# Kernel tuning notes

Measured on AMD Instinct MI355X. Metric: run time of the kernel, lower is better.

The kernel has to match this reference:

```python
import jax, jax.numpy as jnp
import numpy as np

SEQ_LEN = 8192
HIDDEN = 4096
QMAX = 127.0


def _quantize(x_f, scale):
    # per-position requant: round(x / scale), clip to int8 range
    return jnp.clip(jnp.round(x_f / scale[:, None]), -QMAX, QMAX)


def setup_inputs() -> dict:
    key = jax.random.key(0)
    k1, k2, k3, k4 = jax.random.split(key, 4)
    # int8-valued input in [-127, 127]
    x = jax.random.randint(k1, (SEQ_LEN, HIDDEN), -127, 128, dtype=jnp.int32).astype(jnp.int8)
    # per-position scales (calibrated buffers); small positive values typical of int8 activations
    scale_x = jax.random.uniform(k2, (SEQ_LEN,), jnp.float32, 0.01, 0.05)
    scale_y = jax.random.uniform(k3, (SEQ_LEN,), jnp.float32, 0.005, 0.01)  # sigmoid out in (0,1)
    scale_out = jax.random.uniform(k4, (SEQ_LEN,), jnp.float32, 0.01, 0.05)
    return {"x": x, "scale_x": scale_x, "scale_y": scale_y, "scale_out": scale_out}


def reference(x, scale_x, scale_y, scale_out):
    # Quantized SiLU: dequant -> sigmoid -> requant -> dequant both -> mul -> requant
    x_f = x.astype(jnp.float32) * scale_x[:, None]          # [S, H] dequant x
    y_q = _quantize(jax.nn.sigmoid(x_f), scale_y)            # int8-valued sigmoid output
    y_f = y_q * scale_y[:, None]                             # dequant sigmoid output
    out_f = x_f * y_f                                        # elementwise mul in float
    out_q = _quantize(out_f, scale_out).astype(jnp.int8)     # requant to int8
    return out_q, scale_out
```

## Files before the change

kernel.cpp:

```cpp
#include <hip/hip_runtime.h>


#define SEQ_LEN 8192
#define HIDDEN  4096
#define QMAX_F  127.0f

#define VECS_PER_ROW_SHIFT 10
#define TOTAL_VECS ((SEQ_LEN * (long long)HIDDEN) / 4)

__device__ __forceinline__ float silu_q_one(int xi, float s_x, float s_y,
                                            float rcp_none, float s_o) {
    (void)rcp_none;
    float xf  = (float)xi * s_x;
    float e   = expf(-xf);
    float sig = 1.0f / (1.0f + e);
    float yq  = rintf(sig / s_y);
    yq        = fminf(fmaxf(yq, -QMAX_F), QMAX_F);
    float yf  = yq * s_y;
    float of  = xf * yf;
    float oq  = rintf(of / s_o);
    return fminf(fmaxf(oq, -QMAX_F), QMAX_F);
}

__global__ __launch_bounds__(256) void silu_quant_kernel(
    const int*   __restrict__ x,
    const float* __restrict__ scale_x,
    const float* __restrict__ scale_y,
    const float* __restrict__ scale_out,
    float*       __restrict__ out)
{
    const int vid = blockIdx.x * blockDim.x + threadIdx.x;
    if (vid >= (int)TOTAL_VECS) return;
    const int row = vid >> VECS_PER_ROW_SHIFT;

    const float s_x = scale_x[row];
    const float s_y = scale_y[row];
    const float s_o = scale_out[row];

    const int4 xv = ((const int4* __restrict__)x)[vid];

    float4 o;
    o.x = silu_q_one(xv.x, s_x, s_y, 0.f, s_o);
    o.y = silu_q_one(xv.y, s_x, s_y, 0.f, s_o);
    o.z = silu_q_one(xv.z, s_x, s_y, 0.f, s_o);
    o.w = silu_q_one(xv.w, s_x, s_y, 0.f, s_o);

    ((float4* __restrict__)out)[vid] = o;
}

extern "C" void kernel_launch(void* const* d_in, const int* in_sizes, int n_in,
                              void* d_out, int out_size, void* d_ws, size_t ws_size,
                              hipStream_t stream) {
    const int*   x         = (const int*)  d_in[0];
    const float* scale_x   = (const float*)d_in[1];
    const float* scale_y   = (const float*)d_in[2];
    const float* scale_out = (const float*)d_in[3];
    float*       out       = (float*)d_out;

    const int threads = 256;
    const int blocks  = (int)(TOTAL_VECS / threads);
    silu_quant_kernel<<<blocks, threads, 0, stream>>>(x, scale_x, scale_y, scale_out, out);

    hipMemcpyAsync(out + (size_t)SEQ_LEN * HIDDEN, scale_out,
                   SEQ_LEN * sizeof(float), hipMemcpyDeviceToDevice, stream);
}
```

Measured before the change: 228.3 us.

## Process one row per block with nontemporal I/O and fold scale copy into kernel

Restructures the launch so each block handles one row, with every thread processing four vectors. This loads the per-row scales once per block. Global loads and stores use nontemporal builtins, the output-scale divide becomes a multiply by a precomputed reciprocal, and the separate device memcpy of scale_out is folded into the kernel. The reciprocal may change rounding slightly at ties, and the larger per-thread work lowers the block count.

```diff
diff --git a/kernel.cpp b/kernel.cpp
--- a/kernel.cpp
+++ b/kernel.cpp
@@ -4,13 +4,14 @@
 #define SEQ_LEN 8192
 #define HIDDEN  4096
 #define QMAX_F  127.0f
+#define THREADS 256
+#define VECS_PER_THREAD 4
 
-#define VECS_PER_ROW_SHIFT 10
-#define TOTAL_VECS ((SEQ_LEN * (long long)HIDDEN) / 4)
+typedef int   iv4 __attribute__((ext_vector_type(4)));
+typedef float fv4 __attribute__((ext_vector_type(4)));
 
 __device__ __forceinline__ float silu_q_one(int xi, float s_x, float s_y,
-                                            float rcp_none, float s_o) {
-    (void)rcp_none;
+                                            float r_o) {
     float xf  = (float)xi * s_x;
     float e   = expf(-xf);
     float sig = 1.0f / (1.0f + e);
@@ -18,34 +19,41 @@
     yq        = fminf(fmaxf(yq, -QMAX_F), QMAX_F);
     float yf  = yq * s_y;
     float of  = xf * yf;
-    float oq  = rintf(of / s_o);
+    float oq  = rintf(of * r_o);
     return fminf(fmaxf(oq, -QMAX_F), QMAX_F);
 }
 
-__global__ __launch_bounds__(256) void silu_quant_kernel(
+__global__ __launch_bounds__(THREADS) void silu_quant_kernel(
     const int*   __restrict__ x,
     const float* __restrict__ scale_x,
     const float* __restrict__ scale_y,
     const float* __restrict__ scale_out,
     float*       __restrict__ out)
 {
-    const int vid = blockIdx.x * blockDim.x + threadIdx.x;
-    if (vid >= (int)TOTAL_VECS) return;
-    const int row = vid >> VECS_PER_ROW_SHIFT;
+    const int row = blockIdx.x;
 
     const float s_x = scale_x[row];
     const float s_y = scale_y[row];
     const float s_o = scale_out[row];
+    const float r_o = 1.0f / s_o;
 
-    const int4 xv = ((const int4* __restrict__)x)[vid];
+    const iv4* __restrict__ xrow = (const iv4*)(x + (size_t)row * HIDDEN);
+    fv4*       __restrict__ orow = (fv4*)(out + (size_t)row * HIDDEN);
 
-    float4 o;
-    o.x = silu_q_one(xv.x, s_x, s_y, 0.f, s_o);
-    o.y = silu_q_one(xv.y, s_x, s_y, 0.f, s_o);
-    o.z = silu_q_one(xv.z, s_x, s_y, 0.f, s_o);
-    o.w = silu_q_one(xv.w, s_x, s_y, 0.f, s_o);
+    #pragma unroll
+    for (int k = 0; k < VECS_PER_THREAD; ++k) {
+        const int v = threadIdx.x + k * THREADS;
+        iv4 xv = __builtin_nontemporal_load(xrow + v);
+        fv4 o;
+        o.x = silu_q_one(xv.x, s_x, s_y, r_o);
+        o.y = silu_q_one(xv.y, s_x, s_y, r_o);
+        o.z = silu_q_one(xv.z, s_x, s_y, r_o);
+        o.w = silu_q_one(xv.w, s_x, s_y, r_o);
+        __builtin_nontemporal_store(o, orow + v);
+    }
 
-    ((float4* __restrict__)out)[vid] = o;
+    if (threadIdx.x == 0)
+        out[(size_t)SEQ_LEN * HIDDEN + row] = s_o;
 }
 
 extern "C" void kernel_launch(void* const* d_in, const int* in_sizes, int n_in,
@@ -57,10 +65,6 @@
     const float* scale_out = (const float*)d_in[3];
     float*       out       = (float*)d_out;
 
-    const int threads = 256;
-    const int blocks  = (int)(TOTAL_VECS / threads);
-    silu_quant_kernel<<<blocks, threads, 0, stream>>>(x, scale_x, scale_y, scale_out, out);
-
-    hipMemcpyAsync(out + (size_t)SEQ_LEN * HIDDEN, scale_out,
-                   SEQ_LEN * sizeof(float), hipMemcpyDeviceToDevice, stream);
+    silu_quant_kernel<<<SEQ_LEN, THREADS, 0, stream>>>(
+        x, scale_x, scale_y, scale_out, out);
 }
```

After: 226.2 us. Within noise of the previous version (-0.9%).
